# Performance work log

Measured on AMD Instinct MI355X. Metric: run time of the kernel, lower is better.

## Reference

```python
import jax, jax.numpy as jnp
import numpy as np

D_MODEL = 1024
N_HEADS = 16
D_K = D_MODEL // N_HEADS
B, S = 2, 2048


def setup_inputs() -> dict:
    key = jax.random.key(0)
    ks = jax.random.split(key, 5)
    x = jax.random.normal(ks[0], (B, S, D_MODEL), dtype=jnp.float32)
    # causal 0/1 mask, broadcastable over batch and heads
    mask = jnp.tril(jnp.ones((S, S), dtype=jnp.int32))[None, None, :, :]
    scale = 1.0 / np.sqrt(D_MODEL)
    w_qkv_w = jax.random.normal(ks[1], (3 * D_MODEL, D_MODEL), dtype=jnp.float32) * scale
    w_qkv_b = jnp.zeros((3 * D_MODEL,), dtype=jnp.float32)
    w_o_w = jax.random.normal(ks[2], (D_MODEL, D_MODEL), dtype=jnp.float32) * scale
    w_o_b = jnp.zeros((D_MODEL,), dtype=jnp.float32)
    return {"x": x, "mask": mask, "w_qkv_w": w_qkv_w, "w_qkv_b": w_qkv_b,
            "w_o_w": w_o_w, "w_o_b": w_o_b}


def reference(x, mask, w_qkv_w, w_qkv_b, w_o_w, w_o_b):
    b, s, d = x.shape
    qkv = x @ w_qkv_w.T + w_qkv_b                       # [b, s, 3d]
    q, k, v = jnp.split(qkv, 3, axis=-1)
    # [b, h, s, dk]
    q = q.reshape(b, s, N_HEADS, D_K).transpose(0, 2, 1, 3)
    k = k.reshape(b, s, N_HEADS, D_K).transpose(0, 2, 1, 3)
    v = v.reshape(b, s, N_HEADS, D_K).transpose(0, 2, 1, 3)
    scores = jnp.einsum('bhqd,bhkd->bhqk', q, k) / jnp.sqrt(jnp.float32(D_K))
    scores = jnp.where(mask == 0, jnp.float32(-1e9), scores)
    attn = jax.nn.softmax(scores, axis=-1)
    out = jnp.einsum('bhqk,bhkd->bhqd', attn, v)        # [b, h, s, dk]
    out = out.transpose(0, 2, 1, 3).reshape(b, s, d)
    return out @ w_o_w.T + w_o_b
```

## Files before the change

kernel.cpp:

```cpp
#include <hip/hip_runtime.h>
#include <cstdint>
#include <cstddef>


typedef __attribute__((ext_vector_type(8))) short bf16x8;
typedef __attribute__((ext_vector_type(4))) float f32x4;
typedef __attribute__((ext_vector_type(4))) unsigned int u32x4;
typedef __attribute__((ext_vector_type(4))) unsigned short u16x4;
typedef __attribute__((ext_vector_type(8))) unsigned short u16x8;

__device__ __forceinline__ unsigned short f2b(float f) {
  unsigned int u = __float_as_uint(f);
  u = u + 0x7FFFu + ((u >> 16) & 1u);
  return (unsigned short)(u >> 16);
}

__device__ __forceinline__ void gl_lds16(const unsigned short* g, unsigned short* s) {
  __builtin_amdgcn_global_load_lds((const __attribute__((address_space(1))) void*)g,
                                   (__attribute__((address_space(3))) void*)s, 16, 0, 0);
}

__global__ __launch_bounds__(256) void cvt_f32_bf16(const float* __restrict__ in,
                                                    unsigned short* __restrict__ out) {
  const int idx = (blockIdx.x * 256 + threadIdx.x) * 4;
  f32x4 v = *(const f32x4*)(in + idx);
  u16x4 r;
  r[0] = f2b(v[0]); r[1] = f2b(v[1]); r[2] = f2b(v[2]); r[3] = f2b(v[3]);
  *(u16x4*)(out + idx) = r;
}

__global__ __launch_bounds__(256) void gemm_bt(const unsigned short* __restrict__ A,
                                               const unsigned short* __restrict__ W,
                                               const float* __restrict__ bias,
                                               float* __restrict__ Cf,
                                               unsigned short* __restrict__ Cb,
                                               int M, int N, int K) {
  __shared__ unsigned short As[128 * 32];
  __shared__ unsigned short Bs[128 * 32];
  const int tid  = threadIdx.x;
  const int lane = tid & 63;
  const int w    = tid >> 6;
  const int wy   = w >> 1, wx = w & 1;
  const int l15  = lane & 15, quad = lane >> 4;
  const int m0 = blockIdx.y * 128, n0 = blockIdx.x * 128;

  const int c0 = tid, c1 = tid + 256;
  const unsigned short* gA0 = A + (size_t)(m0 + (c0 >> 2)) * K + (c0 & 3) * 8;
  const unsigned short* gA1 = A + (size_t)(m0 + (c1 >> 2)) * K + (c1 & 3) * 8;
  const unsigned short* gB0 = W + (size_t)(n0 + (c0 >> 2)) * K + (c0 & 3) * 8;
  const unsigned short* gB1 = W + (size_t)(n0 + (c1 >> 2)) * K + (c1 & 3) * 8;
  unsigned short* sA0 = &As[c0 * 8];
  unsigned short* sA1 = &As[c1 * 8];
  unsigned short* sB0 = &Bs[c0 * 8];
  unsigned short* sB1 = &Bs[c1 * 8];

  f32x4 acc[4][4];
#pragma unroll
  for (int i = 0; i < 4; ++i)
#pragma unroll
    for (int j = 0; j < 4; ++j) acc[i][j] = (f32x4){0.f, 0.f, 0.f, 0.f};

  for (int kt = 0; kt < K; kt += 32) {
    gl_lds16(gA0 + kt, sA0);
    gl_lds16(gA1 + kt, sA1);
    gl_lds16(gB0 + kt, sB0);
    gl_lds16(gB1 + kt, sB1);
    __syncthreads();
    bf16x8 af[4], bfr[4];
#pragma unroll
    for (int i = 0; i < 4; ++i)
      af[i] = *(const bf16x8*)&As[(wy * 64 + i * 16 + l15) * 32 + quad * 8];
#pragma unroll
    for (int j = 0; j < 4; ++j)
      bfr[j] = *(const bf16x8*)&Bs[(wx * 64 + j * 16 + l15) * 32 + quad * 8];
#pragma unroll
    for (int i = 0; i < 4; ++i)
#pragma unroll
      for (int j = 0; j < 4; ++j)
        acc[i][j] = __builtin_amdgcn_mfma_f32_16x16x32_bf16(af[i], bfr[j], acc[i][j], 0, 0, 0);
    __syncthreads();
  }

#pragma unroll
  for (int i = 0; i < 4; ++i) {
    const int row = m0 + wy * 64 + i * 16 + quad * 4;
#pragma unroll
    for (int j = 0; j < 4; ++j) {
      const int col = n0 + wx * 64 + j * 16 + l15;
      const float bv = bias[col];
#pragma unroll
      for (int r = 0; r < 4; ++r) {
        const float v = acc[i][j][r] + bv;
        if (Cf) Cf[(size_t)(row + r) * N + col] = v;
        else    Cb[(size_t)(row + r) * N + col] = f2b(v);
      }
    }
  }
}

__global__ __launch_bounds__(256) void transpose_v(const unsigned short* __restrict__ qkv,
                                                   unsigned short* __restrict__ vt) {
  __shared__ unsigned short tile[64][72];
  const int tid = threadIdx.x;
  const int bh = blockIdx.y, b = bh >> 4, h = bh & 15;
  const int s0 = blockIdx.x * 64;
  const int i = tid >> 2;
  const int j = (tid & 3) * 16;
  const unsigned short* g = qkv + (size_t)(b * 2048 + s0 + i) * 3072 + 2048 + h * 64 + j;
  *(u32x4*)&tile[i][j]     = *(const u32x4*)g;
  *(u32x4*)&tile[i][j + 8] = *(const u32x4*)(g + 8);
  __syncthreads();
  const int d  = tid >> 2;
  const int sj = (tid & 3) * 16;
  u16x8 o0, o1;
#pragma unroll
  for (int k = 0; k < 8; ++k) { o0[k] = tile[sj + k][d]; o1[k] = tile[sj + 8 + k][d]; }
  unsigned short* gout = vt + (size_t)(bh * 64 + d) * 2048 + s0 + sj;
  *(u16x8*)gout       = o0;
  *(u16x8*)(gout + 8) = o1;
}

__global__ __launch_bounds__(256) void attn_fwd(const unsigned short* __restrict__ qkv,
                                                const unsigned short* __restrict__ vt,
                                                unsigned short* __restrict__ o) {
  __shared__ unsigned short Ks[2][64 * 72];
  __shared__ unsigned short Vs[2][64 * 72];
  __shared__ unsigned short pbuf[4][16 * 72];
  const int tid  = threadIdx.x;
  const int lane = tid & 63;
  const int w    = tid >> 6;
  const int l15  = lane & 15, quad = lane >> 4;
  const int bh = blockIdx.x, b = bh >> 4, h = bh & 15;
  const int qtile = 31 - (int)blockIdx.y;
  const int q0 = qtile * 64 + w * 16;
  const int T = qtile + 1;

  const int srow = tid >> 2;
  const int scol = (tid & 3) * 16;
  const unsigned short* gK = qkv + (size_t)(b * 2048 + srow) * 3072 + 1024 + h * 64 + scol;
  const unsigned short* gV = vt + (size_t)(bh * 64 + srow) * 2048 + scol;

  const unsigned short* qbase = qkv + (size_t)(b * 2048 + q0 + l15) * 3072 + h * 64;
  const bf16x8 aq0 = *(const bf16x8*)(qbase + quad * 8);
  const bf16x8 aq1 = *(const bf16x8*)(qbase + 32 + quad * 8);

  bf16x8 vones;
#pragma unroll
  for (int k = 0; k < 8; ++k) vones[k] = (short)0x3F80;

  f32x4 acc[4];
#pragma unroll
  for (int j = 0; j < 4; ++j) acc[j] = (f32x4){0.f, 0.f, 0.f, 0.f};
  f32x4 accL = (f32x4){0.f, 0.f, 0.f, 0.f};

  unsigned short* P = pbuf[w];

  {
    u32x4 k0 = *(const u32x4*)gK, k1 = *(const u32x4*)(gK + 8);
    u32x4 v0 = *(const u32x4*)gV, v1 = *(const u32x4*)(gV + 8);
    unsigned short* sK = &Ks[0][srow * 72 + scol];
    unsigned short* sV = &Vs[0][srow * 72 + scol];
    *(u32x4*)sK = k0; *(u32x4*)(sK + 8) = k1;
    *(u32x4*)sV = v0; *(u32x4*)(sV + 8) = v1;
  }

  for (int t = 0; t < T; ++t) {
    __syncthreads();
    const int cur = t & 1;
    const unsigned short* Kc = Ks[cur];
    const unsigned short* Vc = Vs[cur];
    u32x4 nk0, nk1, nv0, nv1;
    const bool more = (t + 1 < T);
    if (more) {
      const size_t ko = (size_t)(t + 1) * 64 * 3072;
      const int vo = (t + 1) * 64;
      nk0 = *(const u32x4*)(gK + ko); nk1 = *(const u32x4*)(gK + ko + 8);
      nv0 = *(const u32x4*)(gV + vo); nv1 = *(const u32x4*)(gV + vo + 8);
    }
    const int kv0 = t * 64;
    f32x4 s[4];
#pragma unroll
    for (int n = 0; n < 4; ++n) {
      const bf16x8 bk0 = *(const bf16x8*)&Kc[(n * 16 + l15) * 72 + quad * 8];
      const bf16x8 bk1 = *(const bf16x8*)&Kc[(n * 16 + l15) * 72 + 32 + quad * 8];
      f32x4 z = (f32x4){0.f, 0.f, 0.f, 0.f};
      z = __builtin_amdgcn_mfma_f32_16x16x32_bf16(aq0, bk0, z, 0, 0, 0);
      z = __builtin_amdgcn_mfma_f32_16x16x32_bf16(aq1, bk1, z, 0, 0, 0);
      s[n] = z;
    }
    const bool edge = (kv0 + 63 > q0);
#pragma unroll
    for (int n = 0; n < 4; ++n)
#pragma unroll
      for (int r = 0; r < 4; ++r) {
        float v = s[n][r] * 0.125f;
        if (edge && (kv0 + n * 16 + l15 > q0 + quad * 4 + r)) v = -1e30f;
        s[n][r] = __expf(v);
      }
#pragma unroll
    for (int n = 0; n < 4; ++n)
#pragma unroll
      for (int r = 0; r < 4; ++r)
        P[(quad * 4 + r) * 72 + n * 16 + l15] = f2b(s[n][r]);
    const bf16x8 ap0 = *(const bf16x8*)&P[l15 * 72 + quad * 8];
    const bf16x8 ap1 = *(const bf16x8*)&P[l15 * 72 + 32 + quad * 8];
#pragma unroll
    for (int j = 0; j < 4; ++j) {
      const bf16x8 bv0 = *(const bf16x8*)&Vc[(j * 16 + l15) * 72 + quad * 8];
      const bf16x8 bv1 = *(const bf16x8*)&Vc[(j * 16 + l15) * 72 + 32 + quad * 8];
      acc[j] = __builtin_amdgcn_mfma_f32_16x16x32_bf16(ap0, bv0, acc[j], 0, 0, 0);
      acc[j] = __builtin_amdgcn_mfma_f32_16x16x32_bf16(ap1, bv1, acc[j], 0, 0, 0);
    }
    accL = __builtin_amdgcn_mfma_f32_16x16x32_bf16(ap0, vones, accL, 0, 0, 0);
    accL = __builtin_amdgcn_mfma_f32_16x16x32_bf16(ap1, vones, accL, 0, 0, 0);
    if (more) {
      unsigned short* sK = &Ks[cur ^ 1][srow * 72 + scol];
      unsigned short* sV = &Vs[cur ^ 1][srow * 72 + scol];
      *(u32x4*)sK = nk0; *(u32x4*)(sK + 8) = nk1;
      *(u32x4*)sV = nv0; *(u32x4*)(sV + 8) = nv1;
    }
  }
#pragma unroll
  for (int j = 0; j < 4; ++j)
#pragma unroll
    for (int r = 0; r < 4; ++r) {
      const float v = acc[j][r] / accL[r];
      o[(size_t)(b * 2048 + q0 + quad * 4 + r) * 1024 + h * 64 + j * 16 + l15] = f2b(v);
    }
}

extern "C" void kernel_launch(void* const* d_in, const int* in_sizes, int n_in,
                              void* d_out, int out_size, void* d_ws, size_t ws_size,
                              hipStream_t stream) {
  const float* x       = (const float*)d_in[0];
  const float* w_qkv_w = (const float*)d_in[2];
  const float* w_qkv_b = (const float*)d_in[3];
  const float* w_o_w   = (const float*)d_in[4];
  const float* w_o_b   = (const float*)d_in[5];
  float* out = (float*)d_out;

  unsigned short* ws    = (unsigned short*)d_ws;
  unsigned short* xb    = ws;
  unsigned short* wqb   = xb   + (size_t)4096 * 1024;
  unsigned short* wob   = wqb  + (size_t)3072 * 1024;
  unsigned short* qkvb  = wob  + (size_t)1024 * 1024;
  unsigned short* vtb   = qkvb + (size_t)4096 * 3072;
  unsigned short* attnb = vtb  + (size_t)2048 * 2048;

  cvt_f32_bf16<<<4096, 256, 0, stream>>>(x, xb);
  cvt_f32_bf16<<<3072, 256, 0, stream>>>(w_qkv_w, wqb);
  cvt_f32_bf16<<<1024, 256, 0, stream>>>(w_o_w, wob);
  gemm_bt<<<dim3(24, 32), 256, 0, stream>>>(xb, wqb, w_qkv_b, nullptr, qkvb, 4096, 3072, 1024);
  transpose_v<<<dim3(32, 32), 256, 0, stream>>>(qkvb, vtb);
  attn_fwd<<<dim3(32, 32), 256, 0, stream>>>(qkvb, vtb, attnb);
  gemm_bt<<<dim3(8, 32), 256, 0, stream>>>(attnb, wob, w_o_b, out, nullptr, 4096, 1024, 1024);
}
```

Before: 214.8 us.

## Fuse conversions, fold Q scaling into GEMM, smaller out-proj tiles, pad attention LDS

The three fp32-to-bf16 conversion launches become one fused launch. The 1/sqrt(dk) scale moves into the QKV GEMM epilogue for the Q columns, and causal masking is applied only on edge tiles. A new 64-row-tile GEMM for the output projection doubles its block count to fill more CUs. Attention LDS row pitch changes from 72 to 76 to alter the bank mapping, and P is truncated to bf16 instead of rounded. These cut launch overhead and per-element work, at the risk of slightly different rounding and possibly misaligned 16-byte LDS accesses with the 76 pitch.

```diff
diff --git a/kernel.cpp b/kernel.cpp
--- a/kernel.cpp
+++ b/kernel.cpp
@@ -14,15 +14,29 @@
   u = u + 0x7FFFu + ((u >> 16) & 1u);
   return (unsigned short)(u >> 16);
 }
+__device__ __forceinline__ unsigned short f2b_trunc(float f) {
+  return (unsigned short)(__float_as_uint(f) >> 16);
+}
 
 __device__ __forceinline__ void gl_lds16(const unsigned short* g, unsigned short* s) {
   __builtin_amdgcn_global_load_lds((const __attribute__((address_space(1))) void*)g,
                                    (__attribute__((address_space(3))) void*)s, 16, 0, 0);
 }
 
-__global__ __launch_bounds__(256) void cvt_f32_bf16(const float* __restrict__ in,
-                                                    unsigned short* __restrict__ out) {
-  const int idx = (blockIdx.x * 256 + threadIdx.x) * 4;
+__global__ __launch_bounds__(256) void cvt_all(const float* __restrict__ x,
+                                               const float* __restrict__ wq,
+                                               const float* __restrict__ wo,
+                                               unsigned short* __restrict__ xb,
+                                               unsigned short* __restrict__ wqb,
+                                               unsigned short* __restrict__ wob) {
+  const int bid = blockIdx.x;
+  const float* in;
+  unsigned short* out;
+  int base;
+  if (bid < 4096)      { in = x;  out = xb;  base = bid; }
+  else if (bid < 7168) { in = wq; out = wqb; base = bid - 4096; }
+  else                 { in = wo; out = wob; base = bid - 7168; }
+  const int idx = (base * 256 + threadIdx.x) * 4;
   f32x4 v = *(const f32x4*)(in + idx);
   u16x4 r;
   r[0] = f2b(v[0]); r[1] = f2b(v[1]); r[2] = f2b(v[2]); r[3] = f2b(v[3]);
@@ -32,9 +46,8 @@
 __global__ __launch_bounds__(256) void gemm_bt(const unsigned short* __restrict__ A,
                                                const unsigned short* __restrict__ W,
                                                const float* __restrict__ bias,
-                                               float* __restrict__ Cf,
                                                unsigned short* __restrict__ Cb,
-                                               int M, int N, int K) {
+                                               int M, int N, int K, int qcols) {
   __shared__ unsigned short As[128 * 32];
   __shared__ unsigned short Bs[128 * 32];
   const int tid  = threadIdx.x;
@@ -88,12 +101,72 @@
     for (int j = 0; j < 4; ++j) {
       const int col = n0 + wx * 64 + j * 16 + l15;
       const float bv = bias[col];
-#pragma unroll
-      for (int r = 0; r < 4; ++r) {
-        const float v = acc[i][j][r] + bv;
-        if (Cf) Cf[(size_t)(row + r) * N + col] = v;
-        else    Cb[(size_t)(row + r) * N + col] = f2b(v);
-      }
+      const float sc = (col < qcols) ? 0.125f : 1.0f;
+#pragma unroll
+      for (int r = 0; r < 4; ++r)
+        Cb[(size_t)(row + r) * N + col] = f2b((acc[i][j][r] + bv) * sc);
+    }
+  }
+}
+
+__global__ __launch_bounds__(256) void gemm_bt64(const unsigned short* __restrict__ A,
+                                                 const unsigned short* __restrict__ W,
+                                                 const float* __restrict__ bias,
+                                                 float* __restrict__ Cf,
+                                                 int M, int N, int K) {
+  __shared__ unsigned short As[64 * 32];
+  __shared__ unsigned short Bs[128 * 32];
+  const int tid  = threadIdx.x;
+  const int lane = tid & 63;
+  const int w    = tid >> 6;
+  const int wy   = w >> 1, wx = w & 1;
+  const int l15  = lane & 15, quad = lane >> 4;
+  const int m0 = blockIdx.y * 64, n0 = blockIdx.x * 128;
+
+  const int c0 = tid, c1 = tid + 256;
+  const unsigned short* gA0 = A + (size_t)(m0 + (c0 >> 2)) * K + (c0 & 3) * 8;
+  const unsigned short* gB0 = W + (size_t)(n0 + (c0 >> 2)) * K + (c0 & 3) * 8;
+  const unsigned short* gB1 = W + (size_t)(n0 + (c1 >> 2)) * K + (c1 & 3) * 8;
+  unsigned short* sA0 = &As[c0 * 8];
+  unsigned short* sB0 = &Bs[c0 * 8];
+  unsigned short* sB1 = &Bs[c1 * 8];
+
+  f32x4 acc[2][4];
+#pragma unroll
+  for (int i = 0; i < 2; ++i)
+#pragma unroll
+    for (int j = 0; j < 4; ++j) acc[i][j] = (f32x4){0.f, 0.f, 0.f, 0.f};
+
+  for (int kt = 0; kt < K; kt += 32) {
+    gl_lds16(gA0 + kt, sA0);
+    gl_lds16(gB0 + kt, sB0);
+    gl_lds16(gB1 + kt, sB1);
+    __syncthreads();
+    bf16x8 af[2], bfr[4];
+#pragma unroll
+    for (int i = 0; i < 2; ++i)
+      af[i] = *(const bf16x8*)&As[(wy * 32 + i * 16 + l15) * 32 + quad * 8];
+#pragma unroll
+    for (int j = 0; j < 4; ++j)
+      bfr[j] = *(const bf16x8*)&Bs[(wx * 64 + j * 16 + l15) * 32 + quad * 8];
+#pragma unroll
+    for (int i = 0; i < 2; ++i)
+#pragma unroll
+      for (int j = 0; j < 4; ++j)
+        acc[i][j] = __builtin_amdgcn_mfma_f32_16x16x32_bf16(af[i], bfr[j], acc[i][j], 0, 0, 0);
+    __syncthreads();
+  }
+
+#pragma unroll
+  for (int i = 0; i < 2; ++i) {
+    const int row = m0 + wy * 32 + i * 16 + quad * 4;
+#pragma unroll
+    for (int j = 0; j < 4; ++j) {
+      const int col = n0 + wx * 64 + j * 16 + l15;
+      const float bv = bias[col];
+#pragma unroll
+      for (int r = 0; r < 4; ++r)
+        Cf[(size_t)(row + r) * N + col] = acc[i][j][r] + bv;
     }
   }
 }
@@ -123,9 +196,9 @@
 __global__ __launch_bounds__(256) void attn_fwd(const unsigned short* __restrict__ qkv,
                                                 const unsigned short* __restrict__ vt,
                                                 unsigned short* __restrict__ o) {
-  __shared__ unsigned short Ks[2][64 * 72];
-  __shared__ unsigned short Vs[2][64 * 72];
-  __shared__ unsigned short pbuf[4][16 * 72];
+  __shared__ unsigned short Ks[2][64 * 76];
+  __shared__ unsigned short Vs[2][64 * 76];
+  __shared__ unsigned short pbuf[4][16 * 76];
   const int tid  = threadIdx.x;
   const int lane = tid & 63;
   const int w    = tid >> 6;
@@ -158,8 +231,8 @@
   {
     u32x4 k0 = *(const u32x4*)gK, k1 = *(const u32x4*)(gK + 8);
     u32x4 v0 = *(const u32x4*)gV, v1 = *(const u32x4*)(gV + 8);
-    unsigned short* sK = &Ks[0][srow * 72 + scol];
-    unsigned short* sV = &Vs[0][srow * 72 + scol];
+    unsigned short* sK = &Ks[0][srow * 76 + scol];
+    unsigned short* sV = &Vs[0][srow * 76 + scol];
     *(u32x4*)sK = k0; *(u32x4*)(sK + 8) = k1;
     *(u32x4*)sV = v0; *(u32x4*)(sV + 8) = v1;
   }
@@ -181,41 +254,43 @@
     f32x4 s[4];
 #pragma unroll
     for (int n = 0; n < 4; ++n) {
-      const bf16x8 bk0 = *(const bf16x8*)&Kc[(n * 16 + l15) * 72 + quad * 8];
-      const bf16x8 bk1 = *(const bf16x8*)&Kc[(n * 16 + l15) * 72 + 32 + quad * 8];
+      const bf16x8 bk0 = *(const bf16x8*)&Kc[(n * 16 + l15) * 76 + quad * 8];
+      const bf16x8 bk1 = *(const bf16x8*)&Kc[(n * 16 + l15) * 76 + 32 + quad * 8];
       f32x4 z = (f32x4){0.f, 0.f, 0.f, 0.f};
       z = __builtin_amdgcn_mfma_f32_16x16x32_bf16(aq0, bk0, z, 0, 0, 0);
       z = __builtin_amdgcn_mfma_f32_16x16x32_bf16(aq1, bk1, z, 0, 0, 0);
       s[n] = z;
     }
-    const bool edge = (kv0 + 63 > q0);
+    if (kv0 + 63 > q0) {
+#pragma unroll
+      for (int n = 0; n < 4; ++n)
+#pragma unroll
+        for (int r = 0; r < 4; ++r)
+          if (kv0 + n * 16 + l15 > q0 + quad * 4 + r) s[n][r] = -1e30f;
+    }
 #pragma unroll
     for (int n = 0; n < 4; ++n)
 #pragma unroll
-      for (int r = 0; r < 4; ++r) {
-        float v = s[n][r] * 0.125f;
-        if (edge && (kv0 + n * 16 + l15 > q0 + quad * 4 + r)) v = -1e30f;
-        s[n][r] = __expf(v);
-      }
+      for (int r = 0; r < 4; ++r) s[n][r] = __expf(s[n][r]);
 #pragma unroll
     for (int n = 0; n < 4; ++n)
 #pragma unroll
       for (int r = 0; r < 4; ++r)
-        P[(quad * 4 + r) * 72 + n * 16 + l15] = f2b(s[n][r]);
-    const bf16x8 ap0 = *(const bf16x8*)&P[l15 * 72 + quad * 8];
-    const bf16x8 ap1 = *(const bf16x8*)&P[l15 * 72 + 32 + quad * 8];
+        P[(quad * 4 + r) * 76 + n * 16 + l15] = f2b_trunc(s[n][r]);
+    const bf16x8 ap0 = *(const bf16x8*)&P[l15 * 76 + quad * 8];
+    const bf16x8 ap1 = *(const bf16x8*)&P[l15 * 76 + 32 + quad * 8];
 #pragma unroll
     for (int j = 0; j < 4; ++j) {
-      const bf16x8 bv0 = *(const bf16x8*)&Vc[(j * 16 + l15) * 72 + quad * 8];
-      const bf16x8 bv1 = *(const bf16x8*)&Vc[(j * 16 + l15) * 72 + 32 + quad * 8];
+      const bf16x8 bv0 = *(const bf16x8*)&Vc[(j * 16 + l15) * 76 + quad * 8];
+      const bf16x8 bv1 = *(const bf16x8*)&Vc[(j * 16 + l15) * 76 + 32 + quad * 8];
       acc[j] = __builtin_amdgcn_mfma_f32_16x16x32_bf16(ap0, bv0, acc[j], 0, 0, 0);
       acc[j] = __builtin_amdgcn_mfma_f32_16x16x32_bf16(ap1, bv1, acc[j], 0, 0, 0);
     }
     accL = __builtin_amdgcn_mfma_f32_16x16x32_bf16(ap0, vones, accL, 0, 0, 0);
     accL = __builtin_amdgcn_mfma_f32_16x16x32_bf16(ap1, vones, accL, 0, 0, 0);
     if (more) {
-      unsigned short* sK = &Ks[cur ^ 1][srow * 72 + scol];
-      unsigned short* sV = &Vs[cur ^ 1][srow * 72 + scol];
+      unsigned short* sK = &Ks[cur ^ 1][srow * 76 + scol];
+      unsigned short* sV = &Vs[cur ^ 1][srow * 76 + scol];
       *(u32x4*)sK = nk0; *(u32x4*)(sK + 8) = nk1;
       *(u32x4*)sV = nv0; *(u32x4*)(sV + 8) = nv1;
     }
@@ -247,11 +322,9 @@
   unsigned short* vtb   = qkvb + (size_t)4096 * 3072;
   unsigned short* attnb = vtb  + (size_t)2048 * 2048;
 
-  cvt_f32_bf16<<<4096, 256, 0, stream>>>(x, xb);
-  cvt_f32_bf16<<<3072, 256, 0, stream>>>(w_qkv_w, wqb);
-  cvt_f32_bf16<<<1024, 256, 0, stream>>>(w_o_w, wob);
-  gemm_bt<<<dim3(24, 32), 256, 0, stream>>>(xb, wqb, w_qkv_b, nullptr, qkvb, 4096, 3072, 1024);
+  cvt_all<<<8192, 256, 0, stream>>>(x, w_qkv_w, w_o_w, xb, wqb, wob);
+  gemm_bt<<<dim3(24, 32), 256, 0, stream>>>(xb, wqb, w_qkv_b, qkvb, 4096, 3072, 1024, 1024);
   transpose_v<<<dim3(32, 32), 256, 0, stream>>>(qkvb, vtb);
   attn_fwd<<<dim3(32, 32), 256, 0, stream>>>(qkvb, vtb, attnb);
-  gemm_bt<<<dim3(8, 32), 256, 0, stream>>>(attnb, wob, w_o_b, out, nullptr, 4096, 1024, 1024);
-}
+  gemm_bt64<<<dim3(8, 64), 256, 0, stream>>>(attnb, wob, w_o_b, out, 4096, 1024, 1024);
+}
```

After: 353.5 us. 64.6% more time.
